# Performance work log

Measured on AMD Instinct MI355X. Metric: run time of the kernel, lower is better.

The kernel has to match this reference:

```python
import jax, jax.numpy as jnp
import numpy as np

BS, T, Q, HID, PROJ = 16, 16, 100, 256, 256


def setup_inputs() -> dict:
    key = jax.random.key(0)
    k1, k2, k3, k4, k5 = jax.random.split(key, 5)
    frame_embeds = jax.random.normal(k1, (BS, T, Q, HID), jnp.float32)
    other_frame_embeds = jax.random.normal(k2, (BS, T, Q, HID), jnp.float32)
    W = jax.random.normal(k3, (HID, PROJ), jnp.float32) / np.sqrt(HID).astype(np.float32)
    b = jax.random.normal(k4, (PROJ,), jnp.float32) * 0.01
    n = BS * Q
    mid = jax.random.randint(k5, (n, 1), 1, T - 1, dtype=jnp.int32)
    bridge = jnp.concatenate(
        [jnp.zeros((n, 1), jnp.int32), mid, jnp.full((n, 1), T - 1, jnp.int32)], axis=1
    )  # (n,3): head=0, random pivot in [1,T-2], tail=T-1
    return {"frame_embeds": frame_embeds, "other_frame_embeds": other_frame_embeds,
            "W": W, "b": b, "bridge": bridge}


def _prep(fe, W, b):
    # Linear proj, (bs,t,q,c)->(bs*q, t, c), L2-normalize per embedding.
    bs, t, q, _ = fe.shape
    x = fe @ W + b
    x = x.transpose(0, 2, 1, 3).reshape(bs * q, t, -1)
    return x / jnp.linalg.norm(x, axis=-1, keepdims=True)


def _forward(frame_embeds, other_frame_embeds, W, b, bridge, delta=0.3):
    cur = _prep(frame_embeds, W, b)      # (n,t,c)
    other = _prep(other_frame_embeds, W, b)
    bh = bridge[:, 0].astype(jnp.float32)
    bp_f = bridge[:, 1].astype(jnp.float32)
    bt = bridge[:, 2].astype(jnp.float32)
    alpha = (bp_f - bh) / (bt - bh)      # (n,)
    sigma = alpha * (bt - bp_f)          # (n,)
    g = jnp.take_along_axis(cur, bridge[:, :, None], axis=1)  # (n,3,c) head/pivot/tail
    # positive brownian-bridge distance
    x = g[:, 1] - (1.0 - alpha)[:, None] * g[:, 0] - alpha[:, None] * g[:, 2]
    numer = jnp.exp(-jnp.sum(x * x, axis=-1) / (2.0 * sigma ** 2))  # (n,)
    # negatives: pivot frame taken from every sequence in [cur; other].
    # ||m_ij - a_i||^2 = ||m_ij||^2 - 2 m_ij.a_i + ||a_i||^2 with m_ij = neg_all[j, bp_i],
    # avoiding the (n,N,3,c) repeat tensor of the original.
    neg_all = jnp.concatenate([cur, other], axis=0)            # (N,t,c)
    a = (1.0 - alpha)[:, None] * g[:, 0] + alpha[:, None] * g[:, 2]  # (n,c)
    cross = jnp.einsum('ic,jtc->ijt', a, neg_all)              # (n,N,t)
    bp = bridge[:, 1]
    cross_g = jnp.take_along_axis(cross, bp[:, None, None], axis=2)[..., 0]  # (n,N)
    nn2_g = jnp.sum(neg_all * neg_all, axis=-1).T[bp]          # (n,N)
    x2 = nn2_g - 2.0 * cross_g + jnp.sum(a * a, axis=-1)[:, None]
    dist = -x2 / (2.0 * sigma ** 2)[:, None]                   # (n,N)
    n = dist.shape[0]
    idx = jnp.arange(n)
    self_dist = dist[idx, idx]
    dist = dist.at[idx, idx].set(-10000.0)
    topv, _ = jax.lax.top_k(dist, 5)
    deno = jnp.exp(jnp.concatenate([self_dist[:, None], topv], axis=-1))  # (n,6)
    brownian_loss = (numer / deno.sum(axis=-1)).mean()
    score = jnp.einsum('nc,nc->n', cur[:, 0], cur[:, -1])
    head_tail_match = jax.nn.softplus(delta - score).mean()
    return brownian_loss, head_tail_match


def reference(frame_embeds, other_frame_embeds, W, b, bridge):
    return _forward(frame_embeds, other_frame_embeds, W, b, bridge)
```

## Files before the change

kernel.cpp:

```cpp
#include <hip/hip_runtime.h>
#include <hip/hip_bf16.h>

#define NROW 1600
#define NEG  3200
#define ROWS_FLAT 25600
#define NSPLIT 25

using bf16x8 = __attribute__((ext_vector_type(8))) short;
using f32x4  = __attribute__((ext_vector_type(4))) float;

__device__ __forceinline__ float bf2f(unsigned v) { return __uint_as_float(v << 16); }
__device__ __forceinline__ ushort f2bf(float f) {
  __hip_bfloat16 h = __float2bfloat16(f);
  return *(ushort*)&h;
}
__device__ __forceinline__ float load1(const ushort* p, size_t idx, int f32) {
  return f32 ? ((const float*)p)[idx] : bf2f(p[idx]);
}
__device__ __forceinline__ int sniff_f32(const ushort* p, int lane) {
  unsigned e = ((unsigned)p[2*lane] >> 7) & 0xffu;
  unsigned long long b = __ballot(e >= 100u && e <= 140u);
  return (__popcll(b) >= 40) ? 0 : 1;
}
__device__ __forceinline__ bf16x8 cvt8b(const float* a, const float* b) {
  float4 fa = *(const float4*)a;
  float4 fb = *(const float4*)b;
  bf16x8 r;
  r[0]=(short)f2bf(fa.x); r[1]=(short)f2bf(fa.y); r[2]=(short)f2bf(fa.z); r[3]=(short)f2bf(fa.w);
  r[4]=(short)f2bf(fb.x); r[5]=(short)f2bf(fb.y); r[6]=(short)f2bf(fb.z); r[7]=(short)f2bf(fb.w);
  return r;
}

__global__ __launch_bounds__(256) void k_prep(const ushort* __restrict__ W,
    ushort* __restrict__ Wtf, int* __restrict__ zbase) {
  if (blockIdx.x == 0 && threadIdx.x < 21) zbase[threadIdx.x] = 0;
  int fW = sniff_f32(W, threadIdx.x & 63);
  int n = blockIdx.x, k = threadIdx.x;
  int n16 = n >> 4, m = n & 15, kb = k >> 5, q = (k >> 3) & 3, e = k & 7;
  Wtf[(size_t)(n16*8 + kb)*512 + q*128 + m*8 + e] =
      f2bf(load1(W, (size_t)k * 256 + n, fW));
}

__global__ __launch_bounds__(256) void k_proj(const ushort* __restrict__ fe0,
    const ushort* __restrict__ fe1, const ushort* __restrict__ Wtf,
    const ushort* __restrict__ bias, const int* __restrict__ bridge,
    ushort* __restrict__ Pb, ushort* __restrict__ Ab, float* __restrict__ prm,
    float* __restrict__ numer, int* __restrict__ cnt, int* __restrict__ lst,
    float* __restrict__ wsum) {
  __shared__ union {
    float  xf[32*256];
    ushort x[32*256];
    ushort c[4][32*72];
  } sh;
  __shared__ float s_ss[4][32];
  __shared__ float s_bb[4][2][3];
  __shared__ int   s_brg[2][3];
  const int tid = threadIdx.x;
  const int w = tid >> 6, lane = tid & 63, q = lane >> 4, m = lane & 15;
  const int I0 = blockIdx.x * 2;
  const int hasB = (I0 < NROW);
  const int s1 = (I0 >= NROW);
  const ushort* srcp = s1 ? fe1 : fe0;
  const int fSrc = sniff_f32(srcp, lane);
  const int fB   = sniff_f32(bias, lane);
  if (hasB && tid < 6) s_brg[tid/3][tid%3] = bridge[(I0 + tid/3)*3 + tid%3];
  {
    int ii = I0 - s1*NROW + (w >> 1);
    int b = ii / 100, qq = ii - b*100;
    const size_t ub = (size_t)(b*1600 + qq) * 256;
    if (fSrc) {
      const float* fp = (const float*)srcp;
      #pragma unroll
      for (int i2 = 0; i2 < 8; i2++) {
        int r = w*8 + i2;
        int t = r & 15;
        int g = lane ^ (i2 & 7);
        const float* gp = fp + ub + (size_t)t*25600 + g*4;
        __builtin_amdgcn_global_load_lds(
          (const __attribute__((address_space(1))) unsigned int*)gp,
          (__attribute__((address_space(3))) unsigned int*)&sh.xf[r*256], 16, 0, 0);
      }
    } else {
      #pragma unroll
      for (int i2 = 0; i2 < 4; i2++) {
        int c = w*4 + i2;
        int r  = 2*c + (lane >> 5);
        int t  = r & 15;
        int kc = (lane & 31) ^ (r & 7);
        const ushort* gp = srcp + ub + (size_t)t*25600 + kc*8;
        __builtin_amdgcn_global_load_lds(
          (const __attribute__((address_space(1))) unsigned int*)gp,
          (__attribute__((address_space(3))) unsigned int*)&sh.x[c*512], 16, 0, 0);
      }
    }
  }
  __syncthreads();
  f32x4 acc[2][4];
  #pragma unroll
  for (int nt = 0; nt < 4; nt++) {
    float bb = load1(bias, w*64 + nt*16 + m, fB);
    f32x4 v = {bb, bb, bb, bb};
    #pragma unroll
    for (int mt = 0; mt < 2; mt++) acc[mt][nt] = v;
  }
  const int sw = (m & 7) << 3;
  const ushort* wfb = Wtf + (size_t)(w*4)*4096 + lane*8;
  bf16x8 a_cur[2], b_cur[4];
  if (fSrc) {
    int g0 = (q*2) ^ (m&7), g1 = (q*2 + 1) ^ (m&7);
    #pragma unroll
    for (int mt = 0; mt < 2; mt++)
      a_cur[mt] = cvt8b(&sh.xf[(mt*16+m)*256 + g0*4], &sh.xf[(mt*16+m)*256 + g1*4]);
  } else {
    #pragma unroll
    for (int mt = 0; mt < 2; mt++)
      a_cur[mt] = *(const bf16x8*)&sh.x[(mt*16 + m)*256 + ((q*8) ^ sw)];
  }
  #pragma unroll
  for (int nt = 0; nt < 4; nt++)
    b_cur[nt] = *(const bf16x8*)(wfb + (size_t)nt*4096);
  #pragma unroll
  for (int k = 0; k < 8; k++) {
    bf16x8 a_nxt[2], b_nxt[4];
    if (k < 7) {
      #pragma unroll
      for (int nt = 0; nt < 4; nt++)
        b_nxt[nt] = *(const bf16x8*)(wfb + (size_t)nt*4096 + (k+1)*512);
      if (fSrc) {
        int g0 = ((k+1)*8 + q*2) ^ (m&7), g1 = ((k+1)*8 + q*2 + 1) ^ (m&7);
        #pragma unroll
        for (int mt = 0; mt < 2; mt++)
          a_nxt[mt] = cvt8b(&sh.xf[(mt*16+m)*256 + g0*4], &sh.xf[(mt*16+m)*256 + g1*4]);
      } else {
        int pk = ((k+1)*32 + q*8) ^ sw;
        #pragma unroll
        for (int mt = 0; mt < 2; mt++)
          a_nxt[mt] = *(const bf16x8*)&sh.x[(mt*16 + m)*256 + pk];
      }
    }
    #pragma unroll
    for (int nt = 0; nt < 4; nt++)
      #pragma unroll
      for (int mt = 0; mt < 2; mt++)
        acc[mt][nt] = __builtin_amdgcn_mfma_f32_16x16x32_bf16(a_cur[mt], b_cur[nt], acc[mt][nt], 0, 0, 0);
    if (k < 7) {
      a_cur[0] = a_nxt[0]; a_cur[1] = a_nxt[1];
      #pragma unroll
      for (int x = 0; x < 4; x++) b_cur[x] = b_nxt[x];
    }
  }
  float ssp[2][4];
  #pragma unroll
  for (int mt = 0; mt < 2; mt++)
    #pragma unroll
    for (int reg = 0; reg < 4; reg++) {
      float s = 0.f;
      #pragma unroll
      for (int nt = 0; nt < 4; nt++) { float v = acc[mt][nt][reg]; s += v*v; }
      ssp[mt][reg] = s;
    }
  #pragma unroll
  for (int mk = 1; mk < 16; mk <<= 1)
    #pragma unroll
    for (int mt = 0; mt < 2; mt++)
      #pragma unroll
      for (int reg = 0; reg < 4; reg++) ssp[mt][reg] += __shfl_xor(ssp[mt][reg], mk, 64);
  if (m == 0)
    #pragma unroll
    for (int mt = 0; mt < 2; mt++)
      #pragma unroll
      for (int reg = 0; reg < 4; reg++) s_ss[w][mt*16 + 4*q + reg] = ssp[mt][reg];
  __syncthreads();
  float inv[2][4];
  #pragma unroll
  for (int mt = 0; mt < 2; mt++)
    #pragma unroll
    for (int reg = 0; reg < 4; reg++) {
      int row = mt*16 + 4*q + reg;
      float s = s_ss[0][row] + s_ss[1][row] + s_ss[2][row] + s_ss[3][row];
      inv[mt][reg] = 1.0f / sqrtf(s);
    }
  #pragma unroll
  for (int mt = 0; mt < 2; mt++)
    #pragma unroll
    for (int reg = 0; reg < 4; reg++) {
      int rl = mt*16 + 4*q + reg;
      #pragma unroll
      for (int nt = 0; nt < 4; nt++)
        sh.c[w][rl*72 + nt*16 + m] = f2bf(acc[mt][nt][reg] * inv[mt][reg]);
    }
  __syncthreads();
  #pragma unroll
  for (int j = 0; j < 4; j++) {
    int e   = tid*32 + j*8;
    int r   = e >> 8, col = e & 255;
    uint4 v = *(uint4*)&sh.c[col >> 6][r*72 + (col & 63)];
    *(uint4*)(Pb + (size_t)I0*4096 + e) = v;
  }
  if (hasB) {
    #pragma unroll
    for (int ih = 0; ih < 2; ih++) {
      int bh = s_brg[ih][0], bp = s_brg[ih][1], bt = s_brg[ih][2];
      float alpha = ((float)bp - (float)bh) / ((float)bt - (float)bh);
      int rb = ih*16;
      float g0 = bf2f(sh.c[w][(rb + bh)*72 + lane]);
      float g1 = bf2f(sh.c[w][(rb + bp)*72 + lane]);
      float g2 = bf2f(sh.c[w][(rb + bt)*72 + lane]);
      float hd = bf2f(sh.c[w][(rb +  0)*72 + lane]);
      float tl = bf2f(sh.c[w][(rb + 15)*72 + lane]);
      float a = (1.0f - alpha) * g0 + alpha * g2;
      float x = g1 - a;
      int I = I0 + ih;
      Ab[(size_t)I*256 + w*64 + lane] = f2bf(a);
      float xx = x*x, aa = a*a, sc = hd*tl;
      #pragma unroll
      for (int mk = 1; mk < 64; mk <<= 1) {
        xx += __shfl_xor(xx, mk, 64);
        aa += __shfl_xor(aa, mk, 64);
        sc += __shfl_xor(sc, mk, 64);
      }
      if (lane == 0) { s_bb[w][ih][0] = xx; s_bb[w][ih][1] = aa; s_bb[w][ih][2] = sc; }
    }
    __syncthreads();
    if (tid < 2) {
      int I = I0 + tid;
      float XX = s_bb[0][tid][0] + s_bb[1][tid][0] + s_bb[2][tid][0] + s_bb[3][tid][0];
      float AA = s_bb[0][tid][1] + s_bb[1][tid][1] + s_bb[2][tid][1] + s_bb[3][tid][1];
      float SC = s_bb[0][tid][2] + s_bb[1][tid][2] + s_bb[2][tid][2] + s_bb[3][tid][2];
      int bh = s_brg[tid][0], bp = s_brg[tid][1], bt = s_brg[tid][2];
      float alpha = ((float)bp - (float)bh) / ((float)bt - (float)bh);
      float sigma = alpha * ((float)bt - (float)bp);
      float inv2s2 = 1.0f / (2.0f * sigma * sigma);
      prm[I*2+0] = inv2s2;
      prm[I*2+1] = AA;
      numer[I] = expf(-XX * inv2s2);
      float sp = log1pf(expf(0.3f - SC));
      atomicAdd(wsum + 1, sp * (1.0f / 1600.0f));
      int pos = atomicAdd(cnt + bp, 1);
      lst[bp * 1600 + pos] = I;
    }
  }
}

__device__ __forceinline__ void sort5(float* c) {
  #define CE(i,j) { float hi = fmaxf(c[i], c[j]), lo = fminf(c[i], c[j]); c[i]=hi; c[j]=lo; }
  CE(0,1) CE(3,4) CE(2,4) CE(2,3) CE(1,4) CE(0,3) CE(0,2) CE(1,3) CE(1,2)
  #undef CE
}
__device__ __forceinline__ void ins5(float* t, float v) {
  float hi, lo;
  hi = fmaxf(t[0], v); lo = fminf(t[0], v); t[0] = hi; v = lo;
  hi = fmaxf(t[1], v); lo = fminf(t[1], v); t[1] = hi; v = lo;
  hi = fmaxf(t[2], v); lo = fminf(t[2], v); t[2] = hi; v = lo;
  hi = fmaxf(t[3], v); lo = fminf(t[3], v); t[3] = hi; v = lo;
  t[4] = fmaxf(t[4], v);
}

__global__ __launch_bounds__(256) void k_cross(const ushort* __restrict__ Pb,
    const ushort* __restrict__ Ab, const float* __restrict__ prm,
    const int* __restrict__ cnt, const int* __restrict__ lst,
    float* __restrict__ part) {
  int t = blockIdx.z;
  int n_t = min(cnt[t], 1600);
  int i0 = blockIdx.y * 64;
  if (i0 >= n_t) return;
  int j0 = blockIdx.x * 128;
  __shared__ int s_gis[64];
  __shared__ float s_red[4][64][6];
  int tid = threadIdx.x;
  if (tid < 64) {
    int gi = lst[t*1600 + min(i0 + tid, n_t - 1)];
    s_gis[tid] = min(max(gi, 0), NROW - 1);
  }
  __syncthreads();
  const int w = tid >> 6, lane = tid & 63, q = lane >> 4, m = lane & 15;
  const ushort* jp0 = Pb + ((size_t)(j0 + w*32 + m)*16 + t) * 256 + q*8;
  const ushort* jp1 = jp0 + (size_t)16*16*256;
  int gi[4];
  const ushort* ip[4];
  #pragma unroll
  for (int it = 0; it < 4; it++) {
    gi[it] = s_gis[it*16 + m];
    ip[it] = Ab + (size_t)gi[it] * 256 + q*8;
  }
  f32x4 acc[2][4];
  #pragma unroll
  for (int jt = 0; jt < 2; jt++)
    #pragma unroll
    for (int it = 0; it < 4; it++) { f32x4 z = {0.f,0.f,0.f,0.f}; acc[jt][it] = z; }
  bf16x8 jc0 = *(const bf16x8*)(jp0);
  bf16x8 jc1 = *(const bf16x8*)(jp1);
  bf16x8 ic[4];
  #pragma unroll
  for (int it = 0; it < 4; it++) ic[it] = *(const bf16x8*)(ip[it]);
  #pragma unroll
  for (int k = 0; k < 8; k++) {
    bf16x8 jn0, jn1, in[4];
    if (k < 7) {
      int o = (k + 1) * 32;
      jn0 = *(const bf16x8*)(jp0 + o);
      jn1 = *(const bf16x8*)(jp1 + o);
      #pragma unroll
      for (int it = 0; it < 4; it++) in[it] = *(const bf16x8*)(ip[it] + o);
    }
    __builtin_amdgcn_s_setprio(1);
    #pragma unroll
    for (int it = 0; it < 4; it++) {
      acc[0][it] = __builtin_amdgcn_mfma_f32_16x16x32_bf16(jc0, ic[it], acc[0][it], 0, 0, 0);
      acc[1][it] = __builtin_amdgcn_mfma_f32_16x16x32_bf16(jc1, ic[it], acc[1][it], 0, 0, 0);
    }
    __builtin_amdgcn_s_setprio(0);
    if (k < 7) { jc0 = jn0; jc1 = jn1;
      #pragma unroll
      for (int it = 0; it < 4; it++) ic[it] = in[it];
    }
  }
  float top[4][5], selfv[4];
  float pi[4], pa[4];
  #pragma unroll
  for (int it = 0; it < 4; it++) {
    pi[it] = prm[gi[it]*2]; pa[it] = prm[gi[it]*2+1];
    selfv[it] = -1e30f;
    #pragma unroll
    for (int k = 0; k < 5; k++) top[it][k] = -1e30f;
  }
  #pragma unroll
  for (int jt = 0; jt < 2; jt++)
    #pragma unroll
    for (int reg = 0; reg < 4; reg++) {
      int j = j0 + w*32 + jt*16 + 4*q + reg;
      #pragma unroll
      for (int it = 0; it < 4; it++) {
        float d = -(1.0f - 2.0f*acc[jt][it][reg] + pa[it]) * pi[it];
        if (j == gi[it]) selfv[it] = d; else ins5(top[it], d);
      }
    }
  #pragma unroll
  for (int mk = 16; mk <= 32; mk <<= 1) {
    #pragma unroll
    for (int it = 0; it < 4; it++) {
      float o[5], c[5];
      #pragma unroll
      for (int k = 0; k < 5; k++) o[k] = __shfl_xor(top[it][k], mk, 64);
      #pragma unroll
      for (int k = 0; k < 5; k++) c[k] = fmaxf(top[it][k], o[4 - k]);
      sort5(c);
      #pragma unroll
      for (int k = 0; k < 5; k++) top[it][k] = c[k];
      selfv[it] = fmaxf(selfv[it], __shfl_xor(selfv[it], mk, 64));
    }
  }
  if (q == 0) {
    #pragma unroll
    for (int it = 0; it < 4; it++) {
      #pragma unroll
      for (int k = 0; k < 5; k++) s_red[w][it*16 + m][k] = top[it][k];
      s_red[w][it*16 + m][5] = selfv[it];
    }
  }
  __syncthreads();
  if (tid < 64 && i0 + tid < n_t) {
    float T[5], S = s_red[0][tid][5];
    #pragma unroll
    for (int k = 0; k < 5; k++) T[k] = s_red[0][tid][k];
    #pragma unroll
    for (int w2 = 1; w2 < 4; w2++) {
      #pragma unroll
      for (int k = 0; k < 5; k++) ins5(T, s_red[w2][tid][k]);
      S = fmaxf(S, s_red[w2][tid][5]);
    }
    float* pp = part + ((size_t)s_gis[tid]*NSPLIT + blockIdx.x) * 6;
    #pragma unroll
    for (int k = 0; k < 5; k++) pp[k] = T[k];
    pp[5] = S;
  }
}

__global__ __launch_bounds__(64) void k_merge(const float* __restrict__ part,
    const float* __restrict__ numer, float* __restrict__ wsum, int* __restrict__ done,
    const ushort* __restrict__ fe0, void* __restrict__ out) {
  int i = blockIdx.x * 64 + threadIdx.x;
  const float* pp = part + (size_t)i * NSPLIT * 6;
  float T[5]; float S = pp[5];
  #pragma unroll
  for (int k = 0; k < 5; k++) T[k] = pp[k];
  #pragma unroll
  for (int s = 1; s < NSPLIT; s++) {
    const float* ps = pp + s*6;
    float v0 = ps[0], v1 = ps[1], v2 = ps[2], v3 = ps[3], v4 = ps[4], v5 = ps[5];
    ins5(T, v0); ins5(T, v1); ins5(T, v2); ins5(T, v3); ins5(T, v4);
    S = fmaxf(S, v5);
  }
  float deno = expf(S);
  #pragma unroll
  for (int k = 0; k < 5; k++) deno += expf(T[k]);
  float local = numer[i] / deno;
  #pragma unroll
  for (int mk = 1; mk < 64; mk <<= 1) local += __shfl_xor(local, mk, 64);
  __shared__ int s_last;
  if (threadIdx.x == 0) {
    atomicAdd(wsum + 0, local * (1.0f / 1600.0f));
    __threadfence();
    s_last = (atomicAdd(done, 1) == 24);
  }
  __syncthreads();
  if (s_last) {
    int f = sniff_f32(fe0, threadIdx.x);
    if (threadIdx.x == 0) {
      __threadfence();
      float brown = __hip_atomic_load(wsum + 0, __ATOMIC_RELAXED, __HIP_MEMORY_SCOPE_AGENT);
      float sp    = __hip_atomic_load(wsum + 1, __ATOMIC_RELAXED, __HIP_MEMORY_SCOPE_AGENT);
      if (f) {
        ((float*)out)[0] = brown;
        ((float*)out)[1] = sp;
      } else {
        ushort* o = (ushort*)out;
        o[0] = f2bf(brown);
        o[1] = f2bf(sp);
      }
    }
  }
}

extern "C" void kernel_launch(void* const* d_in, const int* in_sizes, int n_in,
                              void* d_out, int out_size, void* d_ws, size_t ws_size,
                              hipStream_t stream) {
  const ushort* fe0    = (const ushort*)d_in[0];
  const ushort* fe1    = (const ushort*)d_in[1];
  const ushort* W      = (const ushort*)d_in[2];
  const ushort* bias   = (const ushort*)d_in[3];
  const int*    bridge = (const int*)d_in[4];

  ushort* Pb    = (ushort*)d_ws;
  ushort* Ab    = Pb + 13107200;
  ushort* Wtf   = Ab + 409600;
  float*  part  = (float*)(Wtf + 65536);
  float*  prm   = part + 240000;
  float*  numer = prm + 3200;
  float*  wsum  = numer + 1600;
  int*    cnt   = (int*)(wsum + 4);
  int*    done  = cnt + 16;
  int*    lst   = done + 1;

  k_prep  <<<256, 256, 0, stream>>>(W, Wtf, (int*)wsum);
  k_proj  <<<1600, 256, 0, stream>>>(fe0, fe1, Wtf, bias, bridge, Pb, Ab, prm, numer, cnt, lst, wsum);
  k_cross <<<dim3(NSPLIT, 7, 16), 256, 0, stream>>>(Pb, Ab, prm, cnt, lst, part);
  k_merge <<<25, 64, 0, stream>>>(part, numer, wsum, done, fe0, d_out);
}
```

Measured before the change: 161.1 us.

## Stage j-tile in LDS once per block and loop over all row chunks

k_cross now drops the row-chunk grid dimension. Each block copies its 128-row negative tile for one timestep into LDS with direct global-to-LDS loads and an XOR swizzle, then loops over every 64-row chunk of that timestep's list, reading the j operands from LDS. This is meant to stop refetching the same j tile from global memory for each row chunk. In exchange the grid shrinks from 2800 blocks, many of which exit early, to 400. Each block now works through its chunks serially and holds 64KB of LDS, which lowers occupancy and parallelism.

```diff
diff --git a/kernel.cpp b/kernel.cpp
--- a/kernel.cpp
+++ b/kernel.cpp
@@ -260,119 +260,133 @@
     const ushort* __restrict__ Ab, const float* __restrict__ prm,
     const int* __restrict__ cnt, const int* __restrict__ lst,
     float* __restrict__ part) {
-  int t = blockIdx.z;
+  int t = blockIdx.y;
   int n_t = min(cnt[t], 1600);
-  int i0 = blockIdx.y * 64;
-  if (i0 >= n_t) return;
+  if (n_t <= 0) return;
   int j0 = blockIdx.x * 128;
+  __shared__ ushort js[128*256];
   __shared__ int s_gis[64];
   __shared__ float s_red[4][64][6];
   int tid = threadIdx.x;
-  if (tid < 64) {
-    int gi = lst[t*1600 + min(i0 + tid, n_t - 1)];
-    s_gis[tid] = min(max(gi, 0), NROW - 1);
-  }
-  __syncthreads();
   const int w = tid >> 6, lane = tid & 63, q = lane >> 4, m = lane & 15;
-  const ushort* jp0 = Pb + ((size_t)(j0 + w*32 + m)*16 + t) * 256 + q*8;
-  const ushort* jp1 = jp0 + (size_t)16*16*256;
-  int gi[4];
-  const ushort* ip[4];
-  #pragma unroll
-  for (int it = 0; it < 4; it++) {
-    gi[it] = s_gis[it*16 + m];
-    ip[it] = Ab + (size_t)gi[it] * 256 + q*8;
-  }
-  f32x4 acc[2][4];
-  #pragma unroll
-  for (int jt = 0; jt < 2; jt++)
-    #pragma unroll
-    for (int it = 0; it < 4; it++) { f32x4 z = {0.f,0.f,0.f,0.f}; acc[jt][it] = z; }
-  bf16x8 jc0 = *(const bf16x8*)(jp0);
-  bf16x8 jc1 = *(const bf16x8*)(jp1);
-  bf16x8 ic[4];
-  #pragma unroll
-  for (int it = 0; it < 4; it++) ic[it] = *(const bf16x8*)(ip[it]);
-  #pragma unroll
-  for (int k = 0; k < 8; k++) {
-    bf16x8 jn0, jn1, in[4];
-    if (k < 7) {
-      int o = (k + 1) * 32;
-      jn0 = *(const bf16x8*)(jp0 + o);
-      jn1 = *(const bf16x8*)(jp1 + o);
-      #pragma unroll
-      for (int it = 0; it < 4; it++) in[it] = *(const bf16x8*)(ip[it] + o);
-    }
-    __builtin_amdgcn_s_setprio(1);
+  #pragma unroll
+  for (int i2 = 0; i2 < 16; i2++) {
+    int c  = w*16 + i2;
+    int r  = 2*c + (lane >> 5);
+    int kc = (lane & 31) ^ (r & 7);
+    const ushort* gp = Pb + ((size_t)(j0 + r)*16 + t) * 256 + kc*8;
+    __builtin_amdgcn_global_load_lds(
+      (const __attribute__((address_space(1))) unsigned int*)gp,
+      (__attribute__((address_space(3))) unsigned int*)&js[c*512], 16, 0, 0);
+  }
+  const int r0 = w*32 + m, r1 = r0 + 16;
+  const int sz0 = (r0 & 7);
+  for (int i0 = 0; i0 < n_t; i0 += 64) {
+    __syncthreads();
+    if (tid < 64) {
+      int gi = lst[t*1600 + min(i0 + tid, n_t - 1)];
+      s_gis[tid] = min(max(gi, 0), NROW - 1);
+    }
+    __syncthreads();
+    int gi[4];
+    const ushort* ip[4];
     #pragma unroll
     for (int it = 0; it < 4; it++) {
-      acc[0][it] = __builtin_amdgcn_mfma_f32_16x16x32_bf16(jc0, ic[it], acc[0][it], 0, 0, 0);
-      acc[1][it] = __builtin_amdgcn_mfma_f32_16x16x32_bf16(jc1, ic[it], acc[1][it], 0, 0, 0);
-    }
-    __builtin_amdgcn_s_setprio(0);
-    if (k < 7) { jc0 = jn0; jc1 = jn1;
-      #pragma unroll
-      for (int it = 0; it < 4; it++) ic[it] = in[it];
-    }
-  }
-  float top[4][5], selfv[4];
-  float pi[4], pa[4];
-  #pragma unroll
-  for (int it = 0; it < 4; it++) {
-    pi[it] = prm[gi[it]*2]; pa[it] = prm[gi[it]*2+1];
-    selfv[it] = -1e30f;
-    #pragma unroll
-    for (int k = 0; k < 5; k++) top[it][k] = -1e30f;
-  }
-  #pragma unroll
-  for (int jt = 0; jt < 2; jt++)
-    #pragma unroll
-    for (int reg = 0; reg < 4; reg++) {
-      int j = j0 + w*32 + jt*16 + 4*q + reg;
+      gi[it] = s_gis[it*16 + m];
+      ip[it] = Ab + (size_t)gi[it] * 256 + q*8;
+    }
+    f32x4 acc[2][4];
+    #pragma unroll
+    for (int jt = 0; jt < 2; jt++)
+      #pragma unroll
+      for (int it = 0; it < 4; it++) { f32x4 z = {0.f,0.f,0.f,0.f}; acc[jt][it] = z; }
+    bf16x8 jc0 = *(const bf16x8*)&js[r0*256 + ((q + 0) ^ sz0)*8];
+    bf16x8 jc1 = *(const bf16x8*)&js[r1*256 + ((q + 0) ^ sz0)*8];
+    bf16x8 ic[4];
+    #pragma unroll
+    for (int it = 0; it < 4; it++) ic[it] = *(const bf16x8*)(ip[it]);
+    #pragma unroll
+    for (int k = 0; k < 8; k++) {
+      bf16x8 jn0, jn1, in[4];
+      if (k < 7) {
+        int g = (q + 4*(k+1)) ^ sz0;
+        jn0 = *(const bf16x8*)&js[r0*256 + g*8];
+        jn1 = *(const bf16x8*)&js[r1*256 + g*8];
+        int o = (k + 1) * 32;
+        #pragma unroll
+        for (int it = 0; it < 4; it++) in[it] = *(const bf16x8*)(ip[it] + o);
+      }
+      __builtin_amdgcn_s_setprio(1);
       #pragma unroll
       for (int it = 0; it < 4; it++) {
-        float d = -(1.0f - 2.0f*acc[jt][it][reg] + pa[it]) * pi[it];
-        if (j == gi[it]) selfv[it] = d; else ins5(top[it], d);
-      }
-    }
-  #pragma unroll
-  for (int mk = 16; mk <= 32; mk <<= 1) {
+        acc[0][it] = __builtin_amdgcn_mfma_f32_16x16x32_bf16(jc0, ic[it], acc[0][it], 0, 0, 0);
+        acc[1][it] = __builtin_amdgcn_mfma_f32_16x16x32_bf16(jc1, ic[it], acc[1][it], 0, 0, 0);
+      }
+      __builtin_amdgcn_s_setprio(0);
+      if (k < 7) { jc0 = jn0; jc1 = jn1;
+        #pragma unroll
+        for (int it = 0; it < 4; it++) ic[it] = in[it];
+      }
+    }
+    float top[4][5], selfv[4];
+    float pi[4], pa[4];
     #pragma unroll
     for (int it = 0; it < 4; it++) {
-      float o[5], c[5];
-      #pragma unroll
-      for (int k = 0; k < 5; k++) o[k] = __shfl_xor(top[it][k], mk, 64);
-      #pragma unroll
-      for (int k = 0; k < 5; k++) c[k] = fmaxf(top[it][k], o[4 - k]);
-      sort5(c);
-      #pragma unroll
-      for (int k = 0; k < 5; k++) top[it][k] = c[k];
-      selfv[it] = fmaxf(selfv[it], __shfl_xor(selfv[it], mk, 64));
-    }
-  }
-  if (q == 0) {
-    #pragma unroll
-    for (int it = 0; it < 4; it++) {
-      #pragma unroll
-      for (int k = 0; k < 5; k++) s_red[w][it*16 + m][k] = top[it][k];
-      s_red[w][it*16 + m][5] = selfv[it];
-    }
-  }
-  __syncthreads();
-  if (tid < 64 && i0 + tid < n_t) {
-    float T[5], S = s_red[0][tid][5];
-    #pragma unroll
-    for (int k = 0; k < 5; k++) T[k] = s_red[0][tid][k];
-    #pragma unroll
-    for (int w2 = 1; w2 < 4; w2++) {
-      #pragma unroll
-      for (int k = 0; k < 5; k++) ins5(T, s_red[w2][tid][k]);
-      S = fmaxf(S, s_red[w2][tid][5]);
-    }
-    float* pp = part + ((size_t)s_gis[tid]*NSPLIT + blockIdx.x) * 6;
-    #pragma unroll
-    for (int k = 0; k < 5; k++) pp[k] = T[k];
-    pp[5] = S;
+      pi[it] = prm[gi[it]*2]; pa[it] = prm[gi[it]*2+1];
+      selfv[it] = -1e30f;
+      #pragma unroll
+      for (int k = 0; k < 5; k++) top[it][k] = -1e30f;
+    }
+    #pragma unroll
+    for (int jt = 0; jt < 2; jt++)
+      #pragma unroll
+      for (int reg = 0; reg < 4; reg++) {
+        int j = j0 + w*32 + jt*16 + 4*q + reg;
+        #pragma unroll
+        for (int it = 0; it < 4; it++) {
+          float d = -(1.0f - 2.0f*acc[jt][it][reg] + pa[it]) * pi[it];
+          if (j == gi[it]) selfv[it] = d; else ins5(top[it], d);
+        }
+      }
+    #pragma unroll
+    for (int mk = 16; mk <= 32; mk <<= 1) {
+      #pragma unroll
+      for (int it = 0; it < 4; it++) {
+        float o[5], c[5];
+        #pragma unroll
+        for (int k = 0; k < 5; k++) o[k] = __shfl_xor(top[it][k], mk, 64);
+        #pragma unroll
+        for (int k = 0; k < 5; k++) c[k] = fmaxf(top[it][k], o[4 - k]);
+        sort5(c);
+        #pragma unroll
+        for (int k = 0; k < 5; k++) top[it][k] = c[k];
+        selfv[it] = fmaxf(selfv[it], __shfl_xor(selfv[it], mk, 64));
+      }
+    }
+    if (q == 0) {
+      #pragma unroll
+      for (int it = 0; it < 4; it++) {
+        #pragma unroll
+        for (int k = 0; k < 5; k++) s_red[w][it*16 + m][k] = top[it][k];
+        s_red[w][it*16 + m][5] = selfv[it];
+      }
+    }
+    __syncthreads();
+    if (tid < 64 && i0 + tid < n_t) {
+      float T[5], S = s_red[0][tid][5];
+      #pragma unroll
+      for (int k = 0; k < 5; k++) T[k] = s_red[0][tid][k];
+      #pragma unroll
+      for (int w2 = 1; w2 < 4; w2++) {
+        #pragma unroll
+        for (int k = 0; k < 5; k++) ins5(T, s_red[w2][tid][k]);
+        S = fmaxf(S, s_red[w2][tid][5]);
+      }
+      float* pp = part + ((size_t)s_gis[tid]*NSPLIT + blockIdx.x) * 6;
+      #pragma unroll
+      for (int k = 0; k < 5; k++) pp[k] = T[k];
+      pp[5] = S;
+    }
   }
 }
 
@@ -444,6 +458,6 @@
 
   k_prep  <<<256, 256, 0, stream>>>(W, Wtf, (int*)wsum);
   k_proj  <<<1600, 256, 0, stream>>>(fe0, fe1, Wtf, bias, bridge, Pb, Ab, prm, numer, cnt, lst, wsum);
-  k_cross <<<dim3(NSPLIT, 7, 16), 256, 0, stream>>>(Pb, Ab, prm, cnt, lst, part);
+  k_cross <<<dim3(NSPLIT, 16), 256, 0, stream>>>(Pb, Ab, prm, cnt, lst, part);
   k_merge <<<25, 64, 0, stream>>>(part, numer, wsum, done, fe0, d_out);
 }
```

After: 162.5 us. Within noise of the previous version (+0.8%).
